# Kernel tuning notes

Hardware: AMD Instinct MI355X
Metric: run time of the kernel (lower is better)

Reference implementation:

```python
import jax, jax.numpy as jnp
import numpy as np

K_CA3 = 64
HEBBIAN_LR = 1.0
EPS = 1e-10


def kwta(x, k):
    # keep top-k along last dim, zero elsewhere (scatter of top-k values)
    vals, idx = jax.lax.top_k(x, k)
    fx = x.reshape(-1, x.shape[-1])
    fi = idx.reshape(-1, k)
    fv = vals.reshape(-1, k)
    rows = jnp.arange(fx.shape[0])[:, None]
    out = jnp.zeros_like(fx).at[rows, fi].set(fv)
    return out.reshape(x.shape)


def _l2norm(h):
    n = jnp.clip(jnp.linalg.norm(h, axis=-1, keepdims=True), EPS, None)
    return h / n


def setup_inputs() -> dict:
    key = jax.random.key(0)
    ks = jax.random.split(key, 5)
    B, T, D, N = 8, 2048, 512, 2048
    x = jax.random.normal(ks[0], (B, T, D), dtype=jnp.float32)
    # xavier_normal-like scales (gain 0.5 / 0.1), gate small-random for testability
    down_W = jax.random.normal(ks[1], (N, D), dtype=jnp.float32) * (0.5 * np.sqrt(2.0 / (D + N)))
    up_W = jax.random.normal(ks[2], (D, N), dtype=jnp.float32) * (0.1 * np.sqrt(2.0 / (D + N)))
    gate_W = jax.random.normal(ks[3], (D, D), dtype=jnp.float32) * 0.02
    gate_b = jnp.full((D,), -2.0, dtype=jnp.float32)
    return {"x": x, "down_W": down_W, "up_W": up_W, "gate_W": gate_W, "gate_b": gate_b}


def reference(x, down_W, up_W, gate_W, gate_b):
    B, T, D = x.shape
    N = down_W.shape[0]
    # _sparsify: relu -> kWTA -> L2 normalize
    h = jax.nn.relu(jnp.einsum('btd,nd->btn', x, down_W))
    sparse_all = _l2norm(kwta(h, K_CA3))  # (B, T, N)
    # Hebbian fast-weight build (no grad), diagonal masked
    sd = jax.lax.stop_gradient(sparse_all)
    W = HEBBIAN_LR * jnp.einsum('btn,btm->bnm', sd[:, 1:], sd[:, :-1])  # (B, N, N)
    W = W * (1.0 - jnp.eye(N, dtype=W.dtype))
    # retrieval: bmm readback -> relu -> kWTA -> normalize
    succ = jnp.einsum('bnm,btm->btn', W, sparse_all)
    succ = _l2norm(kwta(jax.nn.relu(succ), K_CA3))
    prediction = jnp.einsum('btn,dn->btd', succ, up_W)
    g = jax.nn.sigmoid(jnp.einsum('btd,ed->bte', x, gate_W) + gate_b)
    return x + g * prediction
```

## Files before the change

kernel.cpp:

```cpp
#include <hip/hip_runtime.h>
#include <stdint.h>
#include <math.h>


typedef __attribute__((ext_vector_type(8))) short bf16x8;
typedef __attribute__((ext_vector_type(8))) unsigned short u16x8;
typedef __attribute__((ext_vector_type(8))) unsigned char u8x8;
typedef __attribute__((ext_vector_type(4))) float f32x4;

#define GLD_LDS16(gp, lp)                                     \
  __builtin_amdgcn_global_load_lds(                           \
      (const __attribute__((address_space(1))) void*)(gp),    \
      (__attribute__((address_space(3))) void*)(lp), 16, 0, 0)

__device__ __forceinline__ uint16_t f2bf(float f) {
  uint32_t u = __float_as_uint(f);
  uint32_t r = u + 0x7FFFu + ((u >> 16) & 1u);
  return (uint16_t)(r >> 16);
}
__device__ __forceinline__ float bf2f(unsigned u) {
  return __uint_as_float(u << 16);
}

__device__ __forceinline__ uint8_t f2fp8(float f) {
#if __has_builtin(__builtin_amdgcn_cvt_pk_fp8_f32)
  return (uint8_t)(__builtin_amdgcn_cvt_pk_fp8_f32(f, 0.f, 0, false) & 0xFF);
#else
  if (!(f > 0.f)) return 0;
  if (f >= 448.f) return 0x7E;
  uint32_t u = __float_as_uint(f);
  int e = (int)((u >> 23) & 255) - 127;
  uint32_t m = u & 0x7FFFFFu;
  if (e < -6) {
    float q = f * 512.f;
    int qi = (int)(q + 0.5f);
    if (qi > 7) return 0x08;
    return (uint8_t)qi;
  }
  uint32_t keep = m >> 20;
  uint32_t rem = m & 0xFFFFFu;
  if (rem > 0x80000u || (rem == 0x80000u && (keep & 1))) keep++;
  uint32_t ee = (uint32_t)(e + 7);
  if (keep == 8) { keep = 0; ee++; }
  if (ee >= 16) return 0x7E;
  return (uint8_t)((ee << 3) | keep);
#endif
}

__device__ __forceinline__ int bits_below(unsigned long long m) {
  return __builtin_amdgcn_mbcnt_hi((unsigned)(m >> 32),
                                   __builtin_amdgcn_mbcnt_lo((unsigned)m, 0));
}

__global__ __launch_bounds__(256) void cast_f32_bf16_k(
    const float* __restrict__ s, uint16_t* __restrict__ d, long long n) {
  long long i = (long long)blockIdx.x * 256 + threadIdx.x;
  long long stride = (long long)gridDim.x * 256;
  for (; i < n; i += stride) d[i] = f2bf(s[i]);
}

__global__ __launch_bounds__(256) void zero_f32_k(float* __restrict__ p, long long n) {
  long long i = (long long)blockIdx.x * 256 + threadIdx.x;
  if (i < n) p[i] = 0.f;
}

__global__ __launch_bounds__(256) void transpose_upw_k(
    const float* __restrict__ src, uint16_t* __restrict__ dst, int D, int N) {
  __shared__ float t[32][33];
  int n0 = blockIdx.x * 32, d0 = blockIdx.y * 32;
  int lx = threadIdx.x & 31, ly = threadIdx.x >> 5;
#pragma unroll
  for (int r = 0; r < 4; ++r) {
    int d = d0 + ly + r * 8;
    t[ly + r * 8][lx] = src[(long long)d * N + n0 + lx];
  }
  __syncthreads();
#pragma unroll
  for (int r = 0; r < 4; ++r) {
    int n = n0 + ly + r * 8;
    dst[(long long)n * D + d0 + lx] = f2bf(t[lx][ly + r * 8]);
  }
}

#define EPI_RELU_BF16 0
#define EPI_SIG 2

template <int EPI>
__global__ __launch_bounds__(256) void gemm_bt_k(
    const uint16_t* __restrict__ A, const uint16_t* __restrict__ B,
    void* __restrict__ Cv, const float* __restrict__ bias,
    int M, int N, int K) {
  __shared__ __align__(16) uint16_t As[128 * 32];
  __shared__ __align__(16) uint16_t Bs[128 * 32];
  const int tid = threadIdx.x;
  const int lane = tid & 63;
  const int wave = tid >> 6;
  const int m0 = blockIdx.x * 128;
  const int n0 = blockIdx.y * 128;
  const int wm = (wave & 1) * 64;
  const int wn = (wave >> 1) * 64;
  const int quad = lane >> 4;
  const int l16 = lane & 15;

  f32x4 acc[4][4];
#pragma unroll
  for (int i = 0; i < 4; ++i)
#pragma unroll
    for (int j = 0; j < 4; ++j) acc[i][j] = (f32x4){0.f, 0.f, 0.f, 0.f};

  const int srow = wave * 16 + (lane >> 2);
  const int sseg = lane & 3;
  const long long arow0 = (long long)(m0 + srow) * K + sseg * 8;
  const long long brow0 = (long long)(n0 + srow) * K + sseg * 8;

  for (int k0 = 0; k0 < K; k0 += 32) {
#pragma unroll
    for (int r = 0; r < 2; ++r) {
      GLD_LDS16(A + arow0 + (long long)r * 64 * K + k0,
                &As[(r * 64 + wave * 16) * 32]);
      GLD_LDS16(B + brow0 + (long long)r * 64 * K + k0,
                &Bs[(r * 64 + wave * 16) * 32]);
    }
    __syncthreads();
    bf16x8 af[4], bfr[4];
#pragma unroll
    for (int i = 0; i < 4; ++i)
      af[i] = *(const bf16x8*)(&As[(wm + i * 16 + l16) * 32 + quad * 8]);
#pragma unroll
    for (int j = 0; j < 4; ++j)
      bfr[j] = *(const bf16x8*)(&Bs[(wn + j * 16 + l16) * 32 + quad * 8]);
#pragma unroll
    for (int i = 0; i < 4; ++i)
#pragma unroll
      for (int j = 0; j < 4; ++j)
        acc[i][j] = __builtin_amdgcn_mfma_f32_16x16x32_bf16(af[i], bfr[j], acc[i][j], 0, 0, 0);
    __syncthreads();
  }

#pragma unroll
  for (int i = 0; i < 4; ++i) {
#pragma unroll
    for (int j = 0; j < 4; ++j) {
#pragma unroll
      for (int r = 0; r < 4; ++r) {
        int row = m0 + wm + i * 16 + quad * 4 + r;
        int col = n0 + wn + j * 16 + l16;
        float v = acc[i][j][r];
        if (EPI == EPI_RELU_BF16) {
          uint16_t* C = (uint16_t*)Cv;
          C[(long long)row * N + col] = f2bf(v > 0.f ? v : 0.f);
        } else {
          float* C = (float*)Cv;
          float z = v + bias[col];
          C[(long long)row * N + col] = 1.f / (1.f + __expf(-z));
        }
      }
    }
  }
}

#define RD_AB(KH)                                                              \
  {                                                                            \
    _Pragma("unroll") for (int i = 0; i < 4; ++i) af[i] =                      \
        *(const long*)(la + ((wm + i * 16 + l16) << 6) + koff[KH]);            \
    _Pragma("unroll") for (int j = 0; j < 4; ++j) bfr[j] =                     \
        *(const long*)(lb + ((wn + j * 16 + l16) << 6) + koff[KH]);            \
  }

#define MFMA_4x4()                                                             \
  __builtin_amdgcn_s_setprio(1);                                               \
  _Pragma("unroll") for (int i = 0; i < 4; ++i)                                \
      _Pragma("unroll") for (int j = 0; j < 4; ++j) acc[i][j] =                \
          __builtin_amdgcn_mfma_f32_16x16x32_fp8_fp8(af[i], bfr[j],            \
                                                     acc[i][j], 0, 0, 0);      \
  __builtin_amdgcn_s_setprio(0);

#define STG_ALL()                                                              \
  GLD_LDS16(Ag + (long long)(w * 32 + (lane >> 2)) * 2048 + ko + sc,           \
            sa + w * 2048);                                                    \
  GLD_LDS16(Ag + (long long)(w * 32 + 16 + (lane >> 2)) * 2048 + ko + sc,      \
            sa + w * 2048 + 1024);                                             \
  GLD_LDS16(Bg + (long long)(w * 16 + (lane >> 2)) * 2048 + ko + sc,           \
            sb + w * 1024);

#define FP8_CORE_DECLS_AND_LOOP()                                              \
  const int lane = threadIdx.x & 63;                                           \
  const int w = threadIdx.x >> 6;                                              \
  const int q = lane >> 4, l16 = lane & 15;                                    \
  const int wm = (w >> 1) * 64, wn = (w & 1) * 64;                             \
      \
  const int sc = (((lane & 3) ^ ((lane >> 3) & 3)) << 4);                      \
  f32x4 acc[4][4];                                                             \
  _Pragma("unroll") for (int i = 0; i < 4; ++i)                                \
      _Pragma("unroll") for (int j = 0; j < 4; ++j) acc[i][j] =                \
          (f32x4){0.f, 0.f, 0.f, 0.f};                                         \
  const int Xl = (l16 >> 1) & 3;                                               \
  int koff[2];                                                                 \
  _Pragma("unroll") for (int kh = 0; kh < 2; ++kh) koff[kh] =                  \
      (((kh * 2 + (q >> 1)) ^ Xl) << 4) + (q & 1) * 8;                         \
  {                                                                            \
    uint8_t* sa = &LA[0];                                                      \
    uint8_t* sb = &LB[0];                                                      \
    const int ko = 0;                                                          \
    STG_ALL()                                                                  \
  }                                                                            \
  asm volatile("s_waitcnt vmcnt(0)" ::: "memory");                             \
  __builtin_amdgcn_s_barrier();                                                \
  long af[4], bfr[4];                                                          \
  for (int t = 0; t < 31; ++t) {                                               \
    const int c = t & 1;                                                       \
    const uint8_t* la = &LA[c * 16384];                                        \
    const uint8_t* lb = &LB[c * 8192];                                         \
    uint8_t* sa = &LA[(c ^ 1) * 16384];                                        \
    uint8_t* sb = &LB[(c ^ 1) * 8192];                                         \
    const int ko = (t + 1) * 64;                                               \
    RD_AB(0)                                                                   \
    STG_ALL()                                                                  \
    __builtin_amdgcn_s_barrier();                                              \
    MFMA_4x4()                                                                 \
    __builtin_amdgcn_s_barrier();                                              \
    RD_AB(1)                                                                   \
    __builtin_amdgcn_s_barrier();                                              \
    MFMA_4x4()                                                                 \
    asm volatile("s_waitcnt vmcnt(0)" ::: "memory");                           \
    __builtin_amdgcn_s_barrier();                                              \
  }                                                                            \
  {                                                                            \
    const uint8_t* la = &LA[16384];                                            \
    const uint8_t* lb = &LB[8192];                                             \
    RD_AB(0)                                                                   \
    MFMA_4x4()                                                                 \
    RD_AB(1)                                                                   \
    MFMA_4x4()                                                                 \
  }

__global__ __launch_bounds__(512, 4) void gram_fp8_v2_k(
    const uint8_t* __restrict__ S, uint8_t* __restrict__ G,
    long long sS, long long sG) {
  __shared__ __align__(16) uint8_t LA[32768];
  __shared__ __align__(16) uint8_t LB[16384];
  const int b = blockIdx.z;
  const uint8_t* Sb = S + (long long)b * sS;
  uint8_t* Gb = G + (long long)b * sG;
  int idx = blockIdx.x;
  int ti = 0;
  while ((ti + 1) * (ti + 2) <= idx) ti++;
  const int tj = idx - ti * (ti + 1);
  const int m0 = ti * 256;
  const int n0 = tj * 128;
  const int T = 2048;
  const uint8_t* Ag = Sb + (long long)m0 * 2048;
  const uint8_t* Bg = Sb + (long long)n0 * 2048;

  FP8_CORE_DECLS_AND_LOOP()

  const bool mirror = ((tj >> 1) != ti);
#pragma unroll
  for (int i = 0; i < 4; ++i) {
#pragma unroll
    for (int j = 0; j < 4; ++j) {
      uint8_t bv[4];
#pragma unroll
      for (int r = 0; r < 4; ++r) {
        int row = m0 + wm + i * 16 + q * 4 + r;
        int col = n0 + wn + j * 16 + l16;
        uint8_t h = f2fp8(acc[i][j][r]);
        bv[r] = h;
        Gb[(long long)row * T + col] = h;
      }
      if (mirror) {
        int mrow = n0 + wn + j * 16 + l16;
        int mcol = m0 + wm + i * 16 + q * 4;
        uchar4 pk = {bv[0], bv[1], bv[2], bv[3]};
        *(uchar4*)(&Gb[(long long)mrow * T + mcol]) = pk;
      }
    }
  }
}

__global__ __launch_bounds__(512, 4) void succ_fp8_v2_k(
    const uint8_t* __restrict__ G, const uint8_t* __restrict__ STs,
    uint16_t* __restrict__ C, const float* __restrict__ wd,
    long long sG, long long sB, long long sC) {
  __shared__ __align__(16) uint8_t LA[32768];
  __shared__ __align__(16) uint8_t LB[16384];
  const int b = blockIdx.z;
  const uint8_t* Ab = G + (long long)b * sG;
  const uint8_t* Bb = STs + (long long)b * sB;
  uint16_t* Cb = C + (long long)b * sC;
  const float* wdb = wd + (long long)b * 2048;
  const int m0 = blockIdx.x * 256;
  const int n0 = blockIdx.y * 128;
  const int N = 2048;
  const uint8_t* Ag = Ab + (long long)m0 * 2048;
  const uint8_t* Bg = Bb + (long long)n0 * 2048;

  FP8_CORE_DECLS_AND_LOOP()

#pragma unroll
  for (int i = 0; i < 4; ++i) {
#pragma unroll
    for (int j = 0; j < 4; ++j) {
#pragma unroll
      for (int r = 0; r < 4; ++r) {
        int row = m0 + wm + i * 16 + q * 4 + r;
        int col = n0 + wn + j * 16 + l16;
        long long o = (long long)row * N + col;
        float sv = bf2f(Cb[o]);
        float v = acc[i][j][r] - sv * wdb[col];
        Cb[o] = f2bf(v > 0.f ? v : 0.f);
      }
    }
  }
}

__global__ __launch_bounds__(256) void transpose_shift_wd_k(
    const uint16_t* __restrict__ S, uint8_t* __restrict__ STs,
    float* __restrict__ wd, int T, int N) {
  __shared__ uint16_t tile[65][72];
  __shared__ float wdl[64];
  int t0 = blockIdx.x * 64, n0 = blockIdx.y * 64, b = blockIdx.z;
  const uint16_t* Sb = S + (long long)b * T * N;
  for (int s = threadIdx.x; s < 65 * 8; s += 256) {
    int t = s >> 3, n8 = s & 7;
    u16x8 v = (u16x8){0, 0, 0, 0, 0, 0, 0, 0};
    if (t0 + t < T) v = *(const u16x8*)(Sb + (long long)(t0 + t) * N + n0 + n8 * 8);
    *(u16x8*)(&tile[t][n8 * 8]) = v;
  }
  if (threadIdx.x < 64) wdl[threadIdx.x] = 0.f;
  __syncthreads();
  uint8_t* STsb = STs + (long long)b * N * T;
  for (int s = threadIdx.x; s < 64 * 8; s += 256) {
    int n = s >> 3, t8 = s & 7;
    u8x8 c;
    float part = 0.f;
#pragma unroll
    for (int j = 0; j < 8; ++j) {
      float a = bf2f(tile[t8 * 8 + j][n]);
      float nb = bf2f(tile[t8 * 8 + j + 1][n]);
      c[j] = f2fp8(nb);
      part = fmaf(a, nb, part);
    }
    *(u8x8*)(STsb + (long long)(n0 + n) * T + t0 + t8 * 8) = c;
    atomicAdd(&wdl[n], part);
  }
  __syncthreads();
  if (threadIdx.x < 64)
    atomicAdd(&wd[(long long)b * N + n0 + threadIdx.x], wdl[threadIdx.x]);
}

struct SelInfo {
  unsigned th;
  int cg[4];
  int tc[4];
  int r;
  float inv;
};

__device__ __forceinline__ SelInfo select64(const int k_[4][8],
                                            const u16x8 v[4]) {
  unsigned lo = 0, hi = 0x7FFF;
  while (lo < hi) {
    unsigned mid = (lo + hi) >> 1;
    int cnt = 0;
#pragma unroll
    for (int c = 0; c < 4; ++c)
#pragma unroll
      for (int i = 0; i < 8; ++i)
        cnt += (int)__popcll(__ballot(k_[c][i] > (int)mid));
    if (cnt < 64) hi = mid; else lo = mid + 1;
  }
  SelInfo s;
  s.th = lo;
  const int th = (int)lo;
  int cgt = 0;
#pragma unroll
  for (int c = 0; c < 4; ++c) {
    int cg = 0, tc = 0;
#pragma unroll
    for (int i = 0; i < 8; ++i) {
      cg += (int)__popcll(__ballot(k_[c][i] > th));
      tc += (int)__popcll(__ballot(k_[c][i] == th));
    }
    s.cg[c] = cg;
    s.tc[c] = tc;
    cgt += cg;
  }
  s.r = 64 - cgt;
  float ssq = 0.f;
#pragma unroll
  for (int c = 0; c < 4; ++c)
#pragma unroll
    for (int i = 0; i < 8; ++i)
      if (k_[c][i] > th) {
        float f = bf2f((unsigned)v[c][i]);
        ssq = fmaf(f, f, ssq);
      }
#pragma unroll
  for (int off = 32; off >= 1; off >>= 1) ssq += __shfl_xor(ssq, off, 64);
  float thf = bf2f(lo);
  float sumsq = ssq + (float)s.r * thf * thf;
  s.inv = 1.f / fmaxf(sqrtf(sumsq), 1e-10f);
  return s;
}

__global__ __launch_bounds__(256) void topk1_k(
    const uint16_t* __restrict__ H, uint16_t* __restrict__ Sbf,
    uint8_t* __restrict__ Sf8) {
  const int lane = threadIdx.x & 63;
  const int wave = threadIdx.x >> 6;
  const long long row = (long long)blockIdx.x * 4 + wave;
  const uint16_t* h = H + row * 2048;

  u16x8 v[4];
  int k_[4][8];
#pragma unroll
  for (int c = 0; c < 4; ++c) {
    v[c] = *(const u16x8*)(h + c * 512 + lane * 8);
#pragma unroll
    for (int i = 0; i < 8; ++i) k_[c][i] = (int)v[c][i];
  }
  SelInfo s = select64(k_, v);
  const int th = (int)s.th;

  int tiebase = 0;
#pragma unroll
  for (int c = 0; c < 4; ++c) {
    int B = 0;
#pragma unroll
    for (int j = 0; j < 8; ++j)
      B += bits_below(__ballot(k_[c][j] == th));
    u16x8 o16;
    u8x8 o8;
    int own = 0;
#pragma unroll
    for (int i = 0; i < 8; ++i) {
      int kv = k_[c][i];
      bool ist = (kv == th);
      bool sel = (kv > th) || (ist && (tiebase + B + own) < s.r);
      if (ist) own++;
      float nv = sel ? bf2f((unsigned)v[c][i]) * s.inv : 0.f;
      o16[i] = sel ? (unsigned short)f2bf(nv) : (unsigned short)0;
      o8[i] = sel ? f2fp8(nv) : (uint8_t)0;
    }
    *(u16x8*)(Sbf + row * 2048 + c * 512 + lane * 8) = o16;
    *(u8x8*)(Sf8 + row * 2048 + c * 512 + lane * 8) = o8;
    tiebase += s.tc[c];
  }
}

__global__ __launch_bounds__(256) void topk2_final_k(
    const uint16_t* __restrict__ H, const float* __restrict__ x,
    const float* __restrict__ g, const uint16_t* __restrict__ upTb,
    float* __restrict__ out) {
  const int lane = threadIdx.x & 63;
  const int wave = threadIdx.x >> 6;
  const long long row = (long long)blockIdx.x * 4 + wave;
  const uint16_t* h = H + row * 2048;

  __shared__ int sidx[4][64];
  __shared__ float sval[4][64];

  u16x8 v[4];
  int k_[4][8];
#pragma unroll
  for (int c = 0; c < 4; ++c) {
    v[c] = *(const u16x8*)(h + c * 512 + lane * 8);
#pragma unroll
    for (int i = 0; i < 8; ++i) k_[c][i] = (int)v[c][i];
  }
  SelInfo s = select64(k_, v);
  const int th = (int)s.th;

  int tiebase = 0;
  int cum = 0;
#pragma unroll
  for (int c = 0; c < 4; ++c) {
    int B = 0;
#pragma unroll
    for (int j = 0; j < 8; ++j)
      B += bits_below(__ballot(k_[c][j] == th));
    int own = 0;
#pragma unroll
    for (int i = 0; i < 8; ++i) {
      int kv = k_[c][i];
      bool ist = (kv == th);
      bool sel = (kv > th) || (ist && (tiebase + B + own) < s.r);
      if (ist) own++;
      unsigned long long sm = __ballot(sel);
      if (sel) {
        int slot = cum + bits_below(sm);
        sidx[wave][slot] = c * 512 + lane * 8 + i;
        sval[wave][slot] = bf2f((unsigned)v[c][i]) * s.inv;
      }
      cum += (int)__popcll(sm);
    }
    tiebase += s.tc[c];
  }
  __syncthreads();

  const int col0 = lane * 8;
  float a[8] = {0.f, 0.f, 0.f, 0.f, 0.f, 0.f, 0.f, 0.f};
#pragma unroll 4
  for (int j = 0; j < 64; ++j) {
    int idx = sidx[wave][j];
    float w = sval[wave][j];
    const u16x8 pk = *(const u16x8*)(upTb + (long long)idx * 512 + col0);
#pragma unroll
    for (int q = 0; q < 8; ++q) a[q] = fmaf(w, bf2f((unsigned)pk[q]), a[q]);
  }
  long long o = row * 512 + col0;
  const float4 xv0 = *(const float4*)(x + o);
  const float4 xv1 = *(const float4*)(x + o + 4);
  const float4 gv0 = *(const float4*)(g + o);
  const float4 gv1 = *(const float4*)(g + o + 4);
  float4 r0, r1;
  r0.x = xv0.x + gv0.x * a[0];
  r0.y = xv0.y + gv0.y * a[1];
  r0.z = xv0.z + gv0.z * a[2];
  r0.w = xv0.w + gv0.w * a[3];
  r1.x = xv1.x + gv1.x * a[4];
  r1.y = xv1.y + gv1.y * a[5];
  r1.z = xv1.z + gv1.z * a[6];
  r1.w = xv1.w + gv1.w * a[7];
  *(float4*)(out + o) = r0;
  *(float4*)(out + o + 4) = r1;
}

extern "C" void kernel_launch(void* const* d_in, const int* in_sizes, int n_in,
                              void* d_out, int out_size, void* d_ws, size_t ws_size,
                              hipStream_t stream) {
  const float* x = (const float*)d_in[0];
  const float* downW = (const float*)d_in[1];
  const float* upW = (const float*)d_in[2];
  const float* gateW = (const float*)d_in[3];
  const float* gateB = (const float*)d_in[4];
  float* out = (float*)d_out;

  const int B = 8, T = 2048, D = 512, N = 2048;
  const long long BT = (long long)B * T;
  const long long TN = (long long)T * N;
  const long long TD = (long long)T * D;

  char* base = (char*)d_ws;
  size_t off = 0;
  auto take = [&](size_t bytes) {
    size_t o = off;
    off += (bytes + 255) & ~(size_t)255;
    return o;
  };
  size_t o_xb = take((size_t)BT * D * 2);
  size_t o_dwb = take((size_t)N * D * 2);
  size_t o_gwb = take((size_t)D * D * 2);
  size_t o_upT = take((size_t)N * D * 2);
  const size_t fixed = off;
  const size_t perb = (size_t)TN * 2 + (size_t)TN * 2 + (size_t)TN +
                      (size_t)TN + (size_t)N * 4;
  int Bc = 1;
  if (ws_size >= fixed + 8 * perb) Bc = 8;
  else if (ws_size >= fixed + 4 * perb) Bc = 4;
  else if (ws_size >= fixed + 2 * perb) Bc = 2;

  uint16_t* xb = (uint16_t*)(base + o_xb);
  uint16_t* dwb = (uint16_t*)(base + o_dwb);
  uint16_t* gwb = (uint16_t*)(base + o_gwb);
  uint16_t* upTb = (uint16_t*)(base + o_upT);
  char* p = base + fixed;
  uint16_t* R1 = (uint16_t*)p; p += (size_t)TN * 2 * Bc;
  uint16_t* R2 = (uint16_t*)p; p += (size_t)TN * 2 * Bc;
  uint8_t* R3 = (uint8_t*)p;  p += (size_t)TN * Bc;
  uint8_t* R4 = (uint8_t*)p;  p += (size_t)TN * Bc;
  float* wd = (float*)p;

  cast_f32_bf16_k<<<2048, 256, 0, stream>>>(x, xb, BT * D);
  cast_f32_bf16_k<<<512, 256, 0, stream>>>(downW, dwb, (long long)N * D);
  cast_f32_bf16_k<<<128, 256, 0, stream>>>(gateW, gwb, (long long)D * D);
  transpose_upw_k<<<dim3(N / 32, D / 32), 256, 0, stream>>>(upW, upTb, D, N);

  for (int b0 = 0; b0 < B; b0 += Bc) {
    const uint16_t* xc = xb + (long long)b0 * TD;
    gemm_bt_k<EPI_RELU_BF16><<<dim3(Bc * 16, 16, 1), 256, 0, stream>>>(
        xc, dwb, R1, nullptr, Bc * T, N, D);
    topk1_k<<<Bc * T / 4, 256, 0, stream>>>(R1, R2, R4);
    zero_f32_k<<<(Bc * N + 255) / 256, 256, 0, stream>>>(wd, (long long)Bc * N);
    transpose_shift_wd_k<<<dim3(T / 64, N / 64, Bc), 256, 0, stream>>>(
        R2, R3, wd, T, N);
    gram_fp8_v2_k<<<dim3(72, 1, Bc), 512, 0, stream>>>(
        R4, (uint8_t*)R1, TN, (long long)T * T);
    succ_fp8_v2_k<<<dim3(8, 16, Bc), 512, 0, stream>>>(
        (const uint8_t*)R1, R3, R2, wd, (long long)T * T, TN, TN);
    gemm_bt_k<EPI_SIG><<<dim3(Bc * 16, D / 128, 1), 256, 0, stream>>>(
        xc, gwb, (float*)R3, gateB, Bc * T, D, D);
    topk2_final_k<<<Bc * T / 4, 256, 0, stream>>>(
        R2, x + (long long)b0 * TD, (const float*)R3, upTb,
        out + (long long)b0 * TD);
  }
}
```

Before: 541.0 us.

## Switch gram and succ FP8 GEMMs to MX-scaled 16x16x128 MFMA with 128x128 tiles

Replaces the 16x16x32 fp8 MFMA core of the gram and successor kernels with the gfx950 scaled 16x16x128 f8f6f4 instruction using unit scales (0x7F). The block tile shrinks from 256x128 to 128x128 with 128-wide K steps, a new swizzle, and a two-deep prefetch that waits with partial vmcnt, which roughly doubles the grid. The aim is to cut MFMA issue count and per-K-step barriers. In exchange, each block reuses less data from its tile and the lower-triangle gram indexing and mirror logic have to be rewritten.

```diff
diff --git a/kernel.cpp b/kernel.cpp
--- a/kernel.cpp
+++ b/kernel.cpp
@@ -7,6 +7,8 @@
 typedef __attribute__((ext_vector_type(8))) unsigned short u16x8;
 typedef __attribute__((ext_vector_type(8))) unsigned char u8x8;
 typedef __attribute__((ext_vector_type(4))) float f32x4;
+typedef __attribute__((ext_vector_type(4))) int i32x4;
+typedef __attribute__((ext_vector_type(8))) int i32x8;
 
 #define GLD_LDS16(gp, lp)                                     \
   __builtin_amdgcn_global_load_lds(                           \
@@ -159,104 +161,103 @@
   }
 }
 
-#define RD_AB(KH)                                                              \
-  {                                                                            \
-    _Pragma("unroll") for (int i = 0; i < 4; ++i) af[i] =                      \
-        *(const long*)(la + ((wm + i * 16 + l16) << 6) + koff[KH]);            \
-    _Pragma("unroll") for (int j = 0; j < 4; ++j) bfr[j] =                     \
-        *(const long*)(lb + ((wn + j * 16 + l16) << 6) + koff[KH]);            \
-  }
-
-#define MFMA_4x4()                                                             \
-  __builtin_amdgcn_s_setprio(1);                                               \
-  _Pragma("unroll") for (int i = 0; i < 4; ++i)                                \
-      _Pragma("unroll") for (int j = 0; j < 4; ++j) acc[i][j] =                \
-          __builtin_amdgcn_mfma_f32_16x16x32_fp8_fp8(af[i], bfr[j],            \
-                                                     acc[i][j], 0, 0, 0);      \
-  __builtin_amdgcn_s_setprio(0);
-
-#define STG_ALL()                                                              \
-  GLD_LDS16(Ag + (long long)(w * 32 + (lane >> 2)) * 2048 + ko + sc,           \
-            sa + w * 2048);                                                    \
-  GLD_LDS16(Ag + (long long)(w * 32 + 16 + (lane >> 2)) * 2048 + ko + sc,      \
-            sa + w * 2048 + 1024);                                             \
-  GLD_LDS16(Bg + (long long)(w * 16 + (lane >> 2)) * 2048 + ko + sc,           \
-            sb + w * 1024);
-
-#define FP8_CORE_DECLS_AND_LOOP()                                              \
+__device__ __forceinline__ i32x8 rd32(const uint8_t* base, int o0, int o1) {
+  i32x4 lo = *(const i32x4*)(base + o0);
+  i32x4 hi = *(const i32x4*)(base + o1);
+  i32x8 r;
+  r[0] = lo[0]; r[1] = lo[1]; r[2] = lo[2]; r[3] = lo[3];
+  r[4] = hi[0]; r[5] = hi[1]; r[6] = hi[2]; r[7] = hi[3];
+  return r;
+}
+
+#define MXM(a, b, c) \
+  __builtin_amdgcn_mfma_scale_f32_16x16x128_f8f6f4(a, b, c, 0, 0, 0, 0x7F, 0, 0x7F)
+
+#define STG_TILE(dstA, dstB, KO)                                               \
+  GLD_LDS16(Ag + grow + (KO) + sc0, (dstA) + w * 2048);                        \
+  GLD_LDS16(Ag + grow + 16384 + (KO) + (sc0 ^ 64), (dstA) + w * 2048 + 1024);  \
+  GLD_LDS16(Bg + grow + (KO) + sc0, (dstB) + w * 2048);                        \
+  GLD_LDS16(Bg + grow + 16384 + (KO) + (sc0 ^ 64), (dstB) + w * 2048 + 1024);
+
+#define FP8MX_CORE()                                                           \
   const int lane = threadIdx.x & 63;                                           \
   const int w = threadIdx.x >> 6;                                              \
   const int q = lane >> 4, l16 = lane & 15;                                    \
-  const int wm = (w >> 1) * 64, wn = (w & 1) * 64;                             \
-      \
-  const int sc = (((lane & 3) ^ ((lane >> 3) & 3)) << 4);                      \
-  f32x4 acc[4][4];                                                             \
-  _Pragma("unroll") for (int i = 0; i < 4; ++i)                                \
+  const int wm = (w >> 1) * 32, wn = (w & 1) * 64;                             \
+  const int sc0 = (((lane & 7) ^ (lane >> 4)) << 4);                           \
+  const long long grow = (long long)(w * 16 + (lane >> 3)) * 2048;             \
+  f32x4 acc[2][4];                                                             \
+  _Pragma("unroll") for (int i = 0; i < 2; ++i)                                \
       _Pragma("unroll") for (int j = 0; j < 4; ++j) acc[i][j] =                \
           (f32x4){0.f, 0.f, 0.f, 0.f};                                         \
-  const int Xl = (l16 >> 1) & 3;                                               \
-  int koff[2];                                                                 \
-  _Pragma("unroll") for (int kh = 0; kh < 2; ++kh) koff[kh] =                  \
-      (((kh * 2 + (q >> 1)) ^ Xl) << 4) + (q & 1) * 8;                         \
-  {                                                                            \
-    uint8_t* sa = &LA[0];                                                      \
-    uint8_t* sb = &LB[0];                                                      \
-    const int ko = 0;                                                          \
-    STG_ALL()                                                                  \
-  }                                                                            \
-  asm volatile("s_waitcnt vmcnt(0)" ::: "memory");                             \
+  const int s0 = (((2 * q) ^ (l16 >> 1)) << 4);                                \
+  const int s1 = (((2 * q + 1) ^ (l16 >> 1)) << 4);                            \
+  const int arow0 = (wm + l16) * 128;                                          \
+  const int brow0 = (wn + l16) * 128;                                          \
+  STG_TILE(&LA[0], &LB[0], 0)                                                  \
+  STG_TILE(&LA[16384], &LB[16384], 128)                                        \
+  asm volatile("s_waitcnt vmcnt(4)" ::: "memory");                             \
   __builtin_amdgcn_s_barrier();                                                \
-  long af[4], bfr[4];                                                          \
-  for (int t = 0; t < 31; ++t) {                                               \
+  for (int t = 0; t < 16; ++t) {                                               \
     const int c = t & 1;                                                       \
     const uint8_t* la = &LA[c * 16384];                                        \
-    const uint8_t* lb = &LB[c * 8192];                                         \
-    uint8_t* sa = &LA[(c ^ 1) * 16384];                                        \
-    uint8_t* sb = &LB[(c ^ 1) * 8192];                                         \
-    const int ko = (t + 1) * 64;                                               \
-    RD_AB(0)                                                                   \
-    STG_ALL()                                                                  \
+    const uint8_t* lb = &LB[c * 16384];                                        \
+    i32x8 af0 = rd32(la, arow0 + s0, arow0 + s1);                              \
+    i32x8 af1 = rd32(la, arow0 + 2048 + s0, arow0 + 2048 + s1);                \
+    i32x8 bf0 = rd32(lb, brow0 + s0, brow0 + s1);                              \
+    i32x8 bf1 = rd32(lb, brow0 + 2048 + s0, brow0 + 2048 + s1);                \
+    i32x8 bf2 = rd32(lb, brow0 + 4096 + s0, brow0 + 4096 + s1);                \
+    i32x8 bf3 = rd32(lb, brow0 + 6144 + s0, brow0 + 6144 + s1);                \
+    asm volatile("s_waitcnt lgkmcnt(0)" ::: "memory");                         \
+    __builtin_amdgcn_sched_barrier(0);                                         \
     __builtin_amdgcn_s_barrier();                                              \
-    MFMA_4x4()                                                                 \
-    __builtin_amdgcn_s_barrier();                                              \
-    RD_AB(1)                                                                   \
-    __builtin_amdgcn_s_barrier();                                              \
-    MFMA_4x4()                                                                 \
-    asm volatile("s_waitcnt vmcnt(0)" ::: "memory");                           \
-    __builtin_amdgcn_s_barrier();                                              \
-  }                                                                            \
-  {                                                                            \
-    const uint8_t* la = &LA[16384];                                            \
-    const uint8_t* lb = &LB[8192];                                             \
-    RD_AB(0)                                                                   \
-    MFMA_4x4()                                                                 \
-    RD_AB(1)                                                                   \
-    MFMA_4x4()                                                                 \
-  }
-
-__global__ __launch_bounds__(512, 4) void gram_fp8_v2_k(
+    if (t < 14) {                                                              \
+      const long long ko = (long long)(t + 2) * 128;                           \
+      uint8_t* sa = &LA[c * 16384];                                            \
+      uint8_t* sb = &LB[c * 16384];                                            \
+      STG_TILE(sa, sb, ko)                                                     \
+    }                                                                          \
+    __builtin_amdgcn_s_setprio(1);                                             \
+    acc[0][0] = MXM(af0, bf0, acc[0][0]);                                      \
+    acc[0][1] = MXM(af0, bf1, acc[0][1]);                                      \
+    acc[0][2] = MXM(af0, bf2, acc[0][2]);                                      \
+    acc[0][3] = MXM(af0, bf3, acc[0][3]);                                      \
+    acc[1][0] = MXM(af1, bf0, acc[1][0]);                                      \
+    acc[1][1] = MXM(af1, bf1, acc[1][1]);                                      \
+    acc[1][2] = MXM(af1, bf2, acc[1][2]);                                      \
+    acc[1][3] = MXM(af1, bf3, acc[1][3]);                                      \
+    __builtin_amdgcn_s_setprio(0);                                             \
+    if (t < 14) {                                                              \
+      asm volatile("s_waitcnt vmcnt(4)" ::: "memory");                         \
+    } else if (t == 14) {                                                      \
+      asm volatile("s_waitcnt vmcnt(0)" ::: "memory");                         \
+    }                                                                          \
+    if (t < 15) __builtin_amdgcn_s_barrier();                                  \
+  }
+
+__global__ __launch_bounds__(512, 4) void gram_mx_k(
     const uint8_t* __restrict__ S, uint8_t* __restrict__ G,
     long long sS, long long sG) {
   __shared__ __align__(16) uint8_t LA[32768];
-  __shared__ __align__(16) uint8_t LB[16384];
+  __shared__ __align__(16) uint8_t LB[32768];
   const int b = blockIdx.z;
   const uint8_t* Sb = S + (long long)b * sS;
   uint8_t* Gb = G + (long long)b * sG;
   int idx = blockIdx.x;
   int ti = 0;
-  while ((ti + 1) * (ti + 2) <= idx) ti++;
-  const int tj = idx - ti * (ti + 1);
-  const int m0 = ti * 256;
+  while ((ti + 1) * (ti + 2) / 2 <= idx) ti++;
+  const int tj = idx - ti * (ti + 1) / 2;
+  const int m0 = ti * 128;
   const int n0 = tj * 128;
   const int T = 2048;
   const uint8_t* Ag = Sb + (long long)m0 * 2048;
   const uint8_t* Bg = Sb + (long long)n0 * 2048;
 
-  FP8_CORE_DECLS_AND_LOOP()
-
-  const bool mirror = ((tj >> 1) != ti);
-#pragma unroll
-  for (int i = 0; i < 4; ++i) {
+  FP8MX_CORE()
+
+  const bool mirror = (ti != tj);
+#pragma unroll
+  for (int i = 0; i < 2; ++i) {
 #pragma unroll
     for (int j = 0; j < 4; ++j) {
       uint8_t bv[4];
@@ -278,27 +279,27 @@
   }
 }
 
-__global__ __launch_bounds__(512, 4) void succ_fp8_v2_k(
+__global__ __launch_bounds__(512, 4) void succ_mx_k(
     const uint8_t* __restrict__ G, const uint8_t* __restrict__ STs,
     uint16_t* __restrict__ C, const float* __restrict__ wd,
     long long sG, long long sB, long long sC) {
   __shared__ __align__(16) uint8_t LA[32768];
-  __shared__ __align__(16) uint8_t LB[16384];
+  __shared__ __align__(16) uint8_t LB[32768];
   const int b = blockIdx.z;
   const uint8_t* Ab = G + (long long)b * sG;
   const uint8_t* Bb = STs + (long long)b * sB;
   uint16_t* Cb = C + (long long)b * sC;
   const float* wdb = wd + (long long)b * 2048;
-  const int m0 = blockIdx.x * 256;
+  const int m0 = blockIdx.x * 128;
   const int n0 = blockIdx.y * 128;
   const int N = 2048;
   const uint8_t* Ag = Ab + (long long)m0 * 2048;
   const uint8_t* Bg = Bb + (long long)n0 * 2048;
 
-  FP8_CORE_DECLS_AND_LOOP()
-
-#pragma unroll
-  for (int i = 0; i < 4; ++i) {
+  FP8MX_CORE()
+
+#pragma unroll
+  for (int i = 0; i < 2; ++i) {
 #pragma unroll
     for (int j = 0; j < 4; ++j) {
 #pragma unroll
@@ -585,9 +586,9 @@
     zero_f32_k<<<(Bc * N + 255) / 256, 256, 0, stream>>>(wd, (long long)Bc * N);
     transpose_shift_wd_k<<<dim3(T / 64, N / 64, Bc), 256, 0, stream>>>(
         R2, R3, wd, T, N);
-    gram_fp8_v2_k<<<dim3(72, 1, Bc), 512, 0, stream>>>(
+    gram_mx_k<<<dim3(136, 1, Bc), 512, 0, stream>>>(
         R4, (uint8_t*)R1, TN, (long long)T * T);
-    succ_fp8_v2_k<<<dim3(8, 16, Bc), 512, 0, stream>>>(
+    succ_mx_k<<<dim3(16, 16, Bc), 512, 0, stream>>>(
         (const uint8_t*)R1, R3, R2, wd, (long long)T * T, TN, TN);
     gemm_bt_k<EPI_SIG><<<dim3(Bc * 16, D / 128, 1), 256, 0, stream>>>(
         xc, gwb, (float*)R3, gateB, Bc * T, D, D);
```

Result: slower. 681.1 us (+25.9%).
